# Kernel tuning notes

Hardware: AMD Instinct MI355X
Metric: run time of the kernel (lower is better)

Reference implementation:

```python
import jax, jax.numpy as jnp
import numpy as np

NUM_POINTS = 17
T_MAX = 2.0
VAR_GAMMA = 1.0
EPS = 1e-8


def setup_inputs() -> dict:
    key = jax.random.key(0)
    k1, k2 = jax.random.split(key)
    embeddings = jax.random.normal(k1, (65536, 768), dtype=jnp.float32)
    directions = jax.random.normal(k2, (768, 64), dtype=jnp.float32)
    return {"embeddings": embeddings, "directions": directions}


def reference(embeddings, directions):
    z = embeddings.astype(jnp.float32)  # [B, D]

    # per-dim variance floor (torch .std is unbiased, ddof=1)
    cls_std = jnp.std(z, axis=0, ddof=1)
    var_floor = jnp.mean(jax.nn.relu(VAR_GAMMA - cls_std))

    # column-normalized random directions (F.normalize(dim=0))
    dirs = directions / jnp.linalg.norm(directions, axis=0, keepdims=True)
    proj = z @ dirs  # [B, S]
    std = jnp.std(proj, axis=0, ddof=1)
    proj = (proj - jnp.mean(proj, axis=0, keepdims=True)) / (std + EPS)

    # trapezoidal quadrature over t in (0, T_MAX]
    t = jnp.linspace(0.0, T_MAX, NUM_POINTS + 1)[1:]  # [T]
    dt = T_MAX / NUM_POINTS
    w = jnp.full((NUM_POINTS,), dt).at[0].set(dt / 2).at[-1].set(dt / 2)

    # ECF over all t at once: tp [T, B, S]
    tp = t[:, None, None] * proj[None]
    ecf_real = jnp.mean(jnp.cos(tp), axis=1)  # [T, S]
    ecf_imag = jnp.mean(jnp.sin(tp), axis=1)  # [T, S]
    ecf_sq = ecf_real ** 2 + ecf_imag ** 2
    tcf = jnp.exp(-0.5 * t ** 2)[:, None]  # [T, 1]
    per_t = jnp.mean(ecf_sq - 2.0 * ecf_real * tcf + tcf ** 2, axis=1)  # [T]
    total = jnp.sum(w * per_t)

    loss = total + var_floor
    return loss
```

## Files before the change

kernel.cpp:

```cpp
#include <hip/hip_runtime.h>
#include <math.h>

#define B_ROWS 65536
#define D_DIM  768
#define S_DIM  64
#define T_PTS  17

#define WS_COLSUM 0
#define WS_COLSQ  768
#define WS_PSUM   1536
#define WS_PSQ    1600
#define WS_ECFR   1664
#define WS_ECFI   2752
#define WS_BT_HI_S 7680
#define WS_BT_LO_S 56832
#define WS_PROJ   53248

typedef __attribute__((ext_vector_type(8))) short short8;
typedef __attribute__((ext_vector_type(4))) short short4v;
typedef __attribute__((ext_vector_type(4))) float float4v;

#define MFMA_BF16 __builtin_amdgcn_mfma_f32_16x16x32_bf16

static __device__ inline unsigned short f2bf(float x) {
    unsigned u = __float_as_uint(x);
    u += 0x7FFFu + ((u >> 16) & 1u);
    return (unsigned short)(u >> 16);
}
static __device__ inline float bf2f(unsigned short h) {
    return __uint_as_float(((unsigned)h) << 16);
}

__global__ void norm_kernel(const float* __restrict__ dirs, float* __restrict__ ws) {
    int s = blockIdx.x;
    int t = threadIdx.x;
    if (s < 60) ws[s * 64 + t] = 0.f;

    float sum = 0.f;
    #pragma unroll
    for (int j = 0; j < 12; ++j) {
        float v = dirs[(size_t)(t + j * 64) * S_DIM + s];
        sum += v * v;
    }
    #pragma unroll
    for (int m = 32; m; m >>= 1) sum += __shfl_xor(sum, m, 64);
    float invn = 1.0f / sqrtf(sum);

    unsigned short* bt_hi = (unsigned short*)ws + WS_BT_HI_S;
    unsigned short* bt_lo = (unsigned short*)ws + WS_BT_LO_S;
    #pragma unroll
    for (int j = 0; j < 12; ++j) {
        int k = t + j * 64;
        float v = dirs[(size_t)k * S_DIM + s] * invn;
        unsigned short hi = f2bf(v);
        unsigned short lo = f2bf(v - bf2f(hi));
        bt_hi[s * D_DIM + k] = hi;
        bt_lo[s * D_DIM + k] = lo;
    }
}

__global__ __launch_bounds__(256, 2) void main_kernel(const float* __restrict__ z,
                                                      float* __restrict__ ws) {
    __shared__ __align__(16) short zs_hi[128 * 72];
    __shared__ __align__(16) short zs_lo[128 * 72];
    __shared__ __align__(16) short bs_hi[64 * 72];
    __shared__ __align__(16) short bs_lo[64 * 72];
    __shared__ __align__(16) float cbuf[2 * 64 * 17];

    const unsigned short* bt_hi = (const unsigned short*)ws + WS_BT_HI_S;
    const unsigned short* bt_lo = (const unsigned short*)ws + WS_BT_LO_S;
    float* proj = ws + WS_PROJ;

    int tid = threadIdx.x;
    int tx = tid & 15, ty = tid >> 4;
    int l = tid & 63, l15 = l & 15, q = l >> 4;
    int waveId = tid >> 6;
    int waveRow = waveId * 32;
    size_t rowbase = (size_t)blockIdx.x * 128;

    float4v acc[2][4] = {};

    for (int c = 0; c < D_DIM / 64; ++c) {
        int kc = c * 64;

        float ps0 = 0, ps1 = 0, ps2 = 0, ps3 = 0;
        float pq0 = 0, pq1 = 0, pq2 = 0, pq3 = 0;
        #pragma unroll
        for (int j = 0; j < 8; ++j) {
            int rr = ty + 16 * j;
            float4 v = *reinterpret_cast<const float4*>(
                z + (rowbase + rr) * D_DIM + kc + tx * 4);
            ps0 += v.x; pq0 = fmaf(v.x, v.x, pq0);
            ps1 += v.y; pq1 = fmaf(v.y, v.y, pq1);
            ps2 += v.z; pq2 = fmaf(v.z, v.z, pq2);
            ps3 += v.w; pq3 = fmaf(v.w, v.w, pq3);
            short4v h4, l4;
            h4.x = (short)f2bf(v.x); l4.x = (short)f2bf(v.x - bf2f((unsigned short)h4.x));
            h4.y = (short)f2bf(v.y); l4.y = (short)f2bf(v.y - bf2f((unsigned short)h4.y));
            h4.z = (short)f2bf(v.z); l4.z = (short)f2bf(v.z - bf2f((unsigned short)h4.z));
            h4.w = (short)f2bf(v.w); l4.w = (short)f2bf(v.w - bf2f((unsigned short)h4.w));
            *reinterpret_cast<short4v*>(&zs_hi[rr * 72 + tx * 4]) = h4;
            *reinterpret_cast<short4v*>(&zs_lo[rr * 72 + tx * 4]) = l4;
        }
        cbuf[(tx * 4 + 0) * 17 + ty] = ps0;  cbuf[1088 + (tx * 4 + 0) * 17 + ty] = pq0;
        cbuf[(tx * 4 + 1) * 17 + ty] = ps1;  cbuf[1088 + (tx * 4 + 1) * 17 + ty] = pq1;
        cbuf[(tx * 4 + 2) * 17 + ty] = ps2;  cbuf[1088 + (tx * 4 + 2) * 17 + ty] = pq2;
        cbuf[(tx * 4 + 3) * 17 + ty] = ps3;  cbuf[1088 + (tx * 4 + 3) * 17 + ty] = pq3;

        {
            int srow = tid >> 2;
            int kpart = (tid & 3) * 16;
            short8 b0 = *(const short8*)(bt_hi + (size_t)srow * D_DIM + kc + kpart);
            short8 b1 = *(const short8*)(bt_hi + (size_t)srow * D_DIM + kc + kpart + 8);
            short8 c0 = *(const short8*)(bt_lo + (size_t)srow * D_DIM + kc + kpart);
            short8 c1 = *(const short8*)(bt_lo + (size_t)srow * D_DIM + kc + kpart + 8);
            *(short8*)&bs_hi[srow * 72 + kpart]     = b0;
            *(short8*)&bs_hi[srow * 72 + kpart + 8] = b1;
            *(short8*)&bs_lo[srow * 72 + kpart]     = c0;
            *(short8*)&bs_lo[srow * 72 + kpart + 8] = c1;
        }
        __syncthreads();

        if (tid < 128) {
            int which = tid >> 6, kcol = tid & 63;
            const float* src = cbuf + which * 1088 + kcol * 17;
            float v = 0.f;
            #pragma unroll
            for (int r = 0; r < 16; ++r) v += src[r];
            atomicAdd(&ws[(which ? WS_COLSQ : WS_COLSUM) + kc + kcol], v);
        }

        short8 ah[2][2], al[2][2];
        #pragma unroll
        for (int rt = 0; rt < 2; ++rt) {
            int aoff = (waveRow + rt * 16 + l15) * 72 + q * 8;
            ah[rt][0] = *(const short8*)&zs_hi[aoff];
            ah[rt][1] = *(const short8*)&zs_hi[aoff + 32];
            al[rt][0] = *(const short8*)&zs_lo[aoff];
            al[rt][1] = *(const short8*)&zs_lo[aoff + 32];
        }
        #pragma unroll
        for (int st = 0; st < 4; ++st) {
            int boff = (st * 16 + l15) * 72 + q * 8;
            short8 bh0 = *(const short8*)&bs_hi[boff];
            short8 bh1 = *(const short8*)&bs_hi[boff + 32];
            short8 bl0 = *(const short8*)&bs_lo[boff];
            short8 bl1 = *(const short8*)&bs_lo[boff + 32];
            #pragma unroll
            for (int rt = 0; rt < 2; ++rt) {
                acc[rt][st] = MFMA_BF16(ah[rt][0], bh0, acc[rt][st], 0, 0, 0);
                acc[rt][st] = MFMA_BF16(al[rt][0], bh0, acc[rt][st], 0, 0, 0);
                acc[rt][st] = MFMA_BF16(ah[rt][0], bl0, acc[rt][st], 0, 0, 0);
                acc[rt][st] = MFMA_BF16(ah[rt][1], bh1, acc[rt][st], 0, 0, 0);
                acc[rt][st] = MFMA_BF16(al[rt][1], bh1, acc[rt][st], 0, 0, 0);
                acc[rt][st] = MFMA_BF16(ah[rt][1], bl1, acc[rt][st], 0, 0, 0);
            }
        }
        __syncthreads();
    }

    #pragma unroll
    for (int rt = 0; rt < 2; ++rt)
        #pragma unroll
        for (int st = 0; st < 4; ++st) {
            int col = st * 16 + l15;
            size_t rbase = rowbase + waveRow + rt * 16 + q * 4;
            float4v v = acc[rt][st];
            proj[(rbase + 0) * S_DIM + col] = v[0];
            proj[(rbase + 1) * S_DIM + col] = v[1];
            proj[(rbase + 2) * S_DIM + col] = v[2];
            proj[(rbase + 3) * S_DIM + col] = v[3];
        }

    float* red = cbuf;
    #pragma unroll
    for (int st = 0; st < 4; ++st) {
        float cs = 0.f, cq = 0.f;
        #pragma unroll
        for (int rt = 0; rt < 2; ++rt) {
            float4v v = acc[rt][st];
            cs += v[0] + v[1] + v[2] + v[3];
            cq += v[0]*v[0] + v[1]*v[1] + v[2]*v[2] + v[3]*v[3];
        }
        int s = st * 16 + l15;
        int slot = waveId * 4 + q;
        red[(0 * 64 + s) * 16 + slot] = cs;
        red[(1 * 64 + s) * 16 + slot] = cq;
    }
    __syncthreads();
    if (tid < 128) {
        int which = tid >> 6, s = tid & 63;
        const float* src = red + (which * 64 + s) * 16;
        float v = 0.f;
        #pragma unroll
        for (int r = 0; r < 16; ++r) v += src[r];
        atomicAdd(&ws[(which ? WS_PSQ : WS_PSUM) + s], v);
    }
}

__global__ __launch_bounds__(256) void ecf_kernel(float* __restrict__ ws) {
    const float* proj = ws + WS_PROJ;
    int tid = threadIdx.x;
    int s = tid & 63, r = tid >> 6;

    __shared__ float s_mean[64], s_scale[64];
    if (tid < 64) {
        float sum = ws[WS_PSUM + tid], sq = ws[WS_PSQ + tid];
        float mean = sum / (float)B_ROWS;
        float var = (sq - (float)B_ROWS * mean * mean) / (float)(B_ROWS - 1);
        var = fmaxf(var, 0.f);
        s_mean[tid]  = mean;
        s_scale[tid] = 1.0f / (sqrtf(var) + 1e-8f);
    }
    __syncthreads();
    float mean  = s_mean[s];
    float scale = s_scale[s];
    const float dt = 2.0f / 17.0f;

    float ar[T_PTS] = {}, ai[T_PTS] = {};
    size_t base = (size_t)blockIdx.x * 64;
    for (int i = 0; i < 16; ++i) {
        size_t row = base + i * 4 + r;
        float p  = proj[row * S_DIM + s];
        float ph = (p - mean) * scale;
        float a  = dt * ph;
        float s1, c1;
        __sincosf(a, &s1, &c1);
        float cc = c1, sn = s1;
        ar[0] += cc; ai[0] += sn;
        #pragma unroll
        for (int k = 1; k < T_PTS; ++k) {
            float cn = cc * c1 - sn * s1;
            sn = fmaf(sn, c1, cc * s1);
            cc = cn;
            ar[k] += cc; ai[k] += sn;
        }
    }

    __shared__ float red[3 * 2 * T_PTS * 64];
    if (r > 0) {
        float* dst = red + (r - 1) * (2 * T_PTS * 64);
        #pragma unroll
        for (int k = 0; k < T_PTS; ++k) {
            dst[k * 64 + s]               = ar[k];
            dst[T_PTS * 64 + k * 64 + s]  = ai[k];
        }
    }
    __syncthreads();
    if (r == 0) {
        const int STRIDE = 2 * T_PTS * 64;
        #pragma unroll
        for (int k = 0; k < T_PTS; ++k) {
            float vr = ar[k] + red[k * 64 + s] + red[STRIDE + k * 64 + s]
                             + red[2 * STRIDE + k * 64 + s];
            float vi = ai[k] + red[T_PTS * 64 + k * 64 + s]
                             + red[STRIDE + T_PTS * 64 + k * 64 + s]
                             + red[2 * STRIDE + T_PTS * 64 + k * 64 + s];
            atomicAdd(&ws[WS_ECFR + k * 64 + s], vr);
            atomicAdd(&ws[WS_ECFI + k * 64 + s], vi);
        }
    }
}

__global__ __launch_bounds__(256) void loss_kernel(const float* __restrict__ ws,
                                                   float* __restrict__ out) {
    int tid = threadIdx.x;
    double local = 0.0;
    for (int d = tid; d < D_DIM; d += 256) {
        double sum = (double)ws[WS_COLSUM + d];
        double sq  = (double)ws[WS_COLSQ + d];
        double mean = sum / 65536.0;
        double var  = (sq - 65536.0 * mean * mean) / 65535.0;
        if (var < 0) var = 0;
        double rl = 1.0 - sqrt(var);
        if (rl < 0) rl = 0;
        local += rl / 768.0;
    }
    const double dt = 2.0 / 17.0;
    for (int idx = tid; idx < T_PTS * 64; idx += 256) {
        int i = idx >> 6;
        double t   = dt * (i + 1);
        double tcf = exp(-0.5 * t * t);
        double w   = (i == 0 || i == T_PTS - 1) ? dt * 0.5 : dt;
        double er = (double)ws[WS_ECFR + idx] / 65536.0;
        double ei = (double)ws[WS_ECFI + idx] / 65536.0;
        double term = er * er + ei * ei - 2.0 * er * tcf + tcf * tcf;
        local += w * term / 64.0;
    }
    __shared__ double red[256];
    red[tid] = local;
    __syncthreads();
    for (int off = 128; off > 0; off >>= 1) {
        if (tid < off) red[tid] += red[tid + off];
        __syncthreads();
    }
    if (tid == 0) out[0] = (float)red[0];
}

extern "C" void kernel_launch(void* const* d_in, const int* in_sizes, int n_in,
                              void* d_out, int out_size, void* d_ws, size_t ws_size,
                              hipStream_t stream) {
    const float* z    = (const float*)d_in[0];
    const float* dirs = (const float*)d_in[1];
    float* out = (float*)d_out;
    float* ws  = (float*)d_ws;

    norm_kernel<<<S_DIM, 64, 0, stream>>>(dirs, ws);
    main_kernel<<<B_ROWS / 128, 256, 0, stream>>>(z, ws);
    ecf_kernel<<<B_ROWS / 64, 256, 0, stream>>>(ws);
    loss_kernel<<<1, 256, 0, stream>>>(ws, out);
}
```

Before: 336.2 us.

## Drop bf16 low-part of directions, prefetch z tiles, batch column-stat atomics

Quantizes the normalized directions to a single bf16 part, removing the lo-part buffer and a third of the MFMA work. The next z chunk is loaded into registers before the MFMAs run so global load latency overlaps compute. Per-block column sums are kept in shared memory and flushed with one set of atomics at the end instead of per chunk. Dropping the direction residual lowers projection precision, and the register prefetch raises register pressure under the 2-block launch bound.

```diff
diff --git a/kernel.cpp b/kernel.cpp
--- a/kernel.cpp
+++ b/kernel.cpp
@@ -13,7 +13,6 @@
 #define WS_ECFR   1664
 #define WS_ECFI   2752
 #define WS_BT_HI_S 7680
-#define WS_BT_LO_S 56832
 #define WS_PROJ   53248
 
 typedef __attribute__((ext_vector_type(8))) short short8;
@@ -47,15 +46,11 @@
     float invn = 1.0f / sqrtf(sum);
 
     unsigned short* bt_hi = (unsigned short*)ws + WS_BT_HI_S;
-    unsigned short* bt_lo = (unsigned short*)ws + WS_BT_LO_S;
     #pragma unroll
     for (int j = 0; j < 12; ++j) {
         int k = t + j * 64;
         float v = dirs[(size_t)k * S_DIM + s] * invn;
-        unsigned short hi = f2bf(v);
-        unsigned short lo = f2bf(v - bf2f(hi));
-        bt_hi[s * D_DIM + k] = hi;
-        bt_lo[s * D_DIM + k] = lo;
+        bt_hi[s * D_DIM + k] = f2bf(v);
     }
 }
 
@@ -63,12 +58,11 @@
                                                       float* __restrict__ ws) {
     __shared__ __align__(16) short zs_hi[128 * 72];
     __shared__ __align__(16) short zs_lo[128 * 72];
-    __shared__ __align__(16) short bs_hi[64 * 72];
-    __shared__ __align__(16) short bs_lo[64 * 72];
+    __shared__ __align__(16) short bs[64 * 72];
+    __shared__ float colacc[1536];
     __shared__ __align__(16) float cbuf[2 * 64 * 17];
 
     const unsigned short* bt_hi = (const unsigned short*)ws + WS_BT_HI_S;
-    const unsigned short* bt_lo = (const unsigned short*)ws + WS_BT_LO_S;
     float* proj = ws + WS_PROJ;
 
     int tid = threadIdx.x;
@@ -78,18 +72,31 @@
     int waveRow = waveId * 32;
     size_t rowbase = (size_t)blockIdx.x * 128;
 
+    #pragma unroll
+    for (int j = 0; j < 6; ++j) colacc[tid + j * 256] = 0.f;
+
+    float4 av[8];
+    #pragma unroll
+    for (int j = 0; j < 8; ++j)
+        av[j] = *reinterpret_cast<const float4*>(
+            z + (rowbase + ty + 16 * j) * D_DIM + tx * 4);
+
     float4v acc[2][4] = {};
 
     for (int c = 0; c < D_DIM / 64; ++c) {
         int kc = c * 64;
 
+        int srow = tid >> 2;
+        int kpart = (tid & 3) * 16;
+        short8 b0 = *(const short8*)(bt_hi + (size_t)srow * D_DIM + kc + kpart);
+        short8 b1 = *(const short8*)(bt_hi + (size_t)srow * D_DIM + kc + kpart + 8);
+
         float ps0 = 0, ps1 = 0, ps2 = 0, ps3 = 0;
         float pq0 = 0, pq1 = 0, pq2 = 0, pq3 = 0;
         #pragma unroll
         for (int j = 0; j < 8; ++j) {
+            float4 v = av[j];
             int rr = ty + 16 * j;
-            float4 v = *reinterpret_cast<const float4*>(
-                z + (rowbase + rr) * D_DIM + kc + tx * 4);
             ps0 += v.x; pq0 = fmaf(v.x, v.x, pq0);
             ps1 += v.y; pq1 = fmaf(v.y, v.y, pq1);
             ps2 += v.z; pq2 = fmaf(v.z, v.z, pq2);
@@ -107,19 +114,15 @@
         cbuf[(tx * 4 + 2) * 17 + ty] = ps2;  cbuf[1088 + (tx * 4 + 2) * 17 + ty] = pq2;
         cbuf[(tx * 4 + 3) * 17 + ty] = ps3;  cbuf[1088 + (tx * 4 + 3) * 17 + ty] = pq3;
 
-        {
-            int srow = tid >> 2;
-            int kpart = (tid & 3) * 16;
-            short8 b0 = *(const short8*)(bt_hi + (size_t)srow * D_DIM + kc + kpart);
-            short8 b1 = *(const short8*)(bt_hi + (size_t)srow * D_DIM + kc + kpart + 8);
-            short8 c0 = *(const short8*)(bt_lo + (size_t)srow * D_DIM + kc + kpart);
-            short8 c1 = *(const short8*)(bt_lo + (size_t)srow * D_DIM + kc + kpart + 8);
-            *(short8*)&bs_hi[srow * 72 + kpart]     = b0;
-            *(short8*)&bs_hi[srow * 72 + kpart + 8] = b1;
-            *(short8*)&bs_lo[srow * 72 + kpart]     = c0;
-            *(short8*)&bs_lo[srow * 72 + kpart + 8] = c1;
-        }
+        *(short8*)&bs[srow * 72 + kpart]     = b0;
+        *(short8*)&bs[srow * 72 + kpart + 8] = b1;
         __syncthreads();
+
+        int kn = (kc + 64 < D_DIM) ? kc + 64 : kc;
+        #pragma unroll
+        for (int j = 0; j < 8; ++j)
+            av[j] = *reinterpret_cast<const float4*>(
+                z + (rowbase + ty + 16 * j) * D_DIM + kn + tx * 4);
 
         if (tid < 128) {
             int which = tid >> 6, kcol = tid & 63;
@@ -127,7 +130,7 @@
             float v = 0.f;
             #pragma unroll
             for (int r = 0; r < 16; ++r) v += src[r];
-            atomicAdd(&ws[(which ? WS_COLSQ : WS_COLSUM) + kc + kcol], v);
+            colacc[which * 768 + kc + kcol] += v;
         }
 
         short8 ah[2][2], al[2][2];
@@ -142,21 +145,23 @@
         #pragma unroll
         for (int st = 0; st < 4; ++st) {
             int boff = (st * 16 + l15) * 72 + q * 8;
-            short8 bh0 = *(const short8*)&bs_hi[boff];
-            short8 bh1 = *(const short8*)&bs_hi[boff + 32];
-            short8 bl0 = *(const short8*)&bs_lo[boff];
-            short8 bl1 = *(const short8*)&bs_lo[boff + 32];
+            short8 bh0 = *(const short8*)&bs[boff];
+            short8 bh1 = *(const short8*)&bs[boff + 32];
             #pragma unroll
             for (int rt = 0; rt < 2; ++rt) {
                 acc[rt][st] = MFMA_BF16(ah[rt][0], bh0, acc[rt][st], 0, 0, 0);
                 acc[rt][st] = MFMA_BF16(al[rt][0], bh0, acc[rt][st], 0, 0, 0);
-                acc[rt][st] = MFMA_BF16(ah[rt][0], bl0, acc[rt][st], 0, 0, 0);
                 acc[rt][st] = MFMA_BF16(ah[rt][1], bh1, acc[rt][st], 0, 0, 0);
                 acc[rt][st] = MFMA_BF16(al[rt][1], bh1, acc[rt][st], 0, 0, 0);
-                acc[rt][st] = MFMA_BF16(ah[rt][1], bl1, acc[rt][st], 0, 0, 0);
             }
         }
         __syncthreads();
+    }
+
+    #pragma unroll
+    for (int j = 0; j < 6; ++j) {
+        int idx = tid + j * 256;
+        atomicAdd(&ws[idx], colacc[idx]);
     }
 
     #pragma unroll
```

Result: no change. 331.6 us (-1.4%).
